# Performance work log

Measured on AMD Instinct MI355X. Metric: run time of the kernel, lower is better.

## Reference

```python
import jax, jax.numpy as jnp
import numpy as np

MARGIN = 0.2
EPS = 1e-6  # torch.pairwise_distance default eps added to (x1 - x2)


def setup_inputs() -> dict:
    key = jax.random.key(0)
    k1, k2 = jax.random.split(key)
    N, D = 8192, 128
    x = jax.random.normal(k1, (N, D), dtype=jnp.float32)
    target = jax.random.randint(k2, (N,), 0, 1000)
    return {"x": x, "target": target}


def _pairwise_dist(x):
    # torch.pairwise_distance(x.unsqueeze(0), x.unsqueeze(1)):
    #   diff[i, j] = x[j] - x[i] + EPS ; dist[i, j] = ||diff[i, j]||_2
    # Expanded quadratic form avoids the [N, N, D] diff tensor:
    #   ||a - b + e||^2 = ||a||^2 + ||b||^2 - 2 a.b + 2e*sum(a - b) + D*e^2
    sq = jnp.sum(x * x, axis=1)          # [N]
    s = jnp.sum(x, axis=1)               # [N]
    dot = x @ x.T                        # [N, N]
    D = x.shape[1]
    d2 = (sq[None, :] + sq[:, None] - 2.0 * dot
          + 2.0 * EPS * (s[None, :] - s[:, None]) + D * EPS * EPS)
    return jnp.sqrt(jnp.maximum(d2, 0.0))


def reference(x, target):
    N = x.shape[0]
    dist = _pairwise_dist(x)                                 # [N, N]
    same = target[None, :] == target[:, None]                # [N, N] bool
    pos_mask = (same & ~jnp.eye(N, dtype=bool)).astype(x.dtype)
    hardest_pos = jnp.max(pos_mask * dist, axis=1, keepdims=True)  # [N, 1]
    neg_mask = (~same).astype(x.dtype)
    max_neg = jnp.max(dist, axis=1, keepdims=True)           # [N, 1]
    anchor_neg = dist + max_neg * (1.0 - neg_mask)           # push positives up
    hardest_neg = jnp.min(anchor_neg, axis=1, keepdims=True) # [N, 1]
    loss = jax.nn.relu(hardest_pos - hardest_neg + MARGIN)
    return jnp.mean(loss)
```

## Files before the change

kernel.cpp:

```cpp
#include <hip/hip_runtime.h>

#define N 8192
#define Dk 128
#define EPSC 1e-6f
#define MARGIN 0.2f

typedef __attribute__((ext_vector_type(8))) short bf16x8;
typedef __attribute__((ext_vector_type(4))) float f32x4;

__device__ __forceinline__ unsigned short f2bf(float f) {
    unsigned u = __float_as_uint(f);
    u = (u + 0x7FFFu + ((u >> 16) & 1u)) >> 16;
    return (unsigned short)u;
}
__device__ __forceinline__ unsigned enc(float f) {
    unsigned u = __float_as_uint(f);
    return (u & 0x80000000u) ? ~u : (u | 0x80000000u);
}
__device__ __forceinline__ float dec(unsigned u) {
    return __uint_as_float((u & 0x80000000u) ? (u & 0x7FFFFFFFu) : ~u);
}

__global__ void prep_kernel(const float* __restrict__ x, const int* __restrict__ tgt,
                            unsigned short* __restrict__ Xb, uint2* __restrict__ QT,
                            float* __restrict__ P,
                            unsigned* __restrict__ wsHp, unsigned* __restrict__ wsMn) {
    int row = blockIdx.x * 4 + (threadIdx.x >> 6);
    int l = threadIdx.x & 63;
    const float2 v = *reinterpret_cast<const float2*>(&x[row * Dk + l * 2]);
    float sq = fmaf(v.x, v.x, v.y * v.y);
    float s = v.x + v.y;
    ushort2 a;
    a.x = f2bf(v.x);
    a.y = f2bf(v.y);
    *reinterpret_cast<ushort2*>(&Xb[row * Dk + l * 2]) = a;
#pragma unroll
    for (int m = 32; m >= 1; m >>= 1) {
        sq += __shfl_xor(sq, m);
        s += __shfl_xor(s, m);
    }
    if (l == 0) {
        P[row] = sq - 2.0f * EPSC * s;
        float Qj = sq + 2.0f * EPSC * s + (float)Dk * EPSC * EPSC;
        uint2 qt;
        qt.x = __float_as_uint(-0.5f * Qj);
        qt.y = (unsigned)tgt[row];
        QT[row] = qt;
        wsHp[row] = 0xFF800000u;
        wsMn[row] = 0x007FFFFFu;
    }
}

__global__ __launch_bounds__(256, 2) void main_kernel(
        const unsigned short* __restrict__ Xb,
        const uint2* __restrict__ QT, const int* __restrict__ tgt,
        unsigned* __restrict__ wsHp, unsigned* __restrict__ wsMn) {
    const int tid = threadIdx.x;
    const int w = tid >> 6;
    const int lane = tid & 63;
    const int n = lane & 15;
    const int q = lane >> 4;
    const int wi = w >> 1;
    const int wj = w & 1;

    const int ig = (int)blockIdx.x >> 3;
    const int js = (int)blockIdx.x & 7;
    const int rbase = ig * 128 + 64 * wi;

    const bf16x8* Xv = reinterpret_cast<const bf16x8*>(Xb);

    bf16x8 Af[4][4];
#pragma unroll
    for (int ti = 0; ti < 4; ++ti)
#pragma unroll
        for (int kk = 0; kk < 4; ++kk)
            Af[ti][kk] = Xv[(rbase + 16 * ti + n) * 16 + (q + 4 * kk)];

    int tsl[16];
#pragma unroll
    for (int ti = 0; ti < 4; ++ti) {
        int4 t4 = *reinterpret_cast<const int4*>(&tgt[rbase + 16 * ti + 4 * q]);
        tsl[4 * ti + 0] = t4.x;
        tsl[4 * ti + 1] = t4.y;
        tsl[4 * ti + 2] = t4.z;
        tsl[4 * ti + 3] = t4.w;
    }

    float hp[16], mn[16];
#pragma unroll
    for (int s = 0; s < 16; ++s) {
        hp[s] = INFINITY;
        mn[s] = -INFINITY;
    }

    for (int step = 0; step < 8; ++step) {
        const int jbase = js * 1024 + step * 128;

        float Qv[4];
        int tv[4];
#pragma unroll
        for (int tj = 0; tj < 4; ++tj) {
            uint2 qt = QT[jbase + 64 * wj + 16 * tj + n];
            Qv[tj] = __uint_as_float(qt.x);
            tv[tj] = (int)qt.y;
        }

        f32x4 acc[4][4];
#pragma unroll
        for (int ti = 0; ti < 4; ++ti)
#pragma unroll
            for (int tj = 0; tj < 4; ++tj) acc[ti][tj] = Qv[tj];

#pragma unroll
        for (int kk = 0; kk < 4; ++kk) {
            bf16x8 Bf[4];
#pragma unroll
            for (int tj = 0; tj < 4; ++tj)
                Bf[tj] = Xv[(jbase + 64 * wj + 16 * tj + n) * 16 + (q + 4 * kk)];
#pragma unroll
            for (int ti = 0; ti < 4; ++ti)
#pragma unroll
                for (int tj = 0; tj < 4; ++tj)
                    acc[ti][tj] = __builtin_amdgcn_mfma_f32_16x16x32_bf16(Af[ti][kk], Bf[tj],
                                                                          acc[ti][tj], 0, 0, 0);
        }

#pragma unroll
        for (int tj = 0; tj < 4; ++tj) {
            int tvv = tv[tj];
#pragma unroll
            for (int ti = 0; ti < 4; ++ti) {
                f32x4 v = acc[ti][tj];
                int e0 = tvv == tsl[4 * ti + 0];
                int e1 = tvv == tsl[4 * ti + 1];
                int e2 = tvv == tsl[4 * ti + 2];
                int e3 = tvv == tsl[4 * ti + 3];
                if (__ballot(e0 | e1 | e2 | e3)) {
                    hp[4 * ti + 0] = fminf(hp[4 * ti + 0], e0 ? v[0] : INFINITY);
                    hp[4 * ti + 1] = fminf(hp[4 * ti + 1], e1 ? v[1] : INFINITY);
                    hp[4 * ti + 2] = fminf(hp[4 * ti + 2], e2 ? v[2] : INFINITY);
                    hp[4 * ti + 3] = fminf(hp[4 * ti + 3], e3 ? v[3] : INFINITY);
                    mn[4 * ti + 0] = fmaxf(mn[4 * ti + 0], e0 ? -INFINITY : v[0]);
                    mn[4 * ti + 1] = fmaxf(mn[4 * ti + 1], e1 ? -INFINITY : v[1]);
                    mn[4 * ti + 2] = fmaxf(mn[4 * ti + 2], e2 ? -INFINITY : v[2]);
                    mn[4 * ti + 3] = fmaxf(mn[4 * ti + 3], e3 ? -INFINITY : v[3]);
                } else {
                    mn[4 * ti + 0] = fmaxf(mn[4 * ti + 0], v[0]);
                    mn[4 * ti + 1] = fmaxf(mn[4 * ti + 1], v[1]);
                    mn[4 * ti + 2] = fmaxf(mn[4 * ti + 2], v[2]);
                    mn[4 * ti + 3] = fmaxf(mn[4 * ti + 3], v[3]);
                }
            }
        }
    }

#pragma unroll
    for (int m = 1; m <= 8; m <<= 1) {
#pragma unroll
        for (int s = 0; s < 16; ++s) {
            hp[s] = fminf(hp[s], __shfl_xor(hp[s], m));
            mn[s] = fmaxf(mn[s], __shfl_xor(mn[s], m));
        }
    }
    if (n == 0) {
#pragma unroll
        for (int ti = 0; ti < 4; ++ti) {
#pragma unroll
            for (int r = 0; r < 4; ++r) {
                int i = rbase + 16 * ti + 4 * q + r;
                atomicMin(&wsHp[i], enc(hp[4 * ti + r]));
                atomicMax(&wsMn[i], enc(mn[4 * ti + r]));
            }
        }
    }
}

__global__ void finish_kernel(const float* __restrict__ P,
                              const unsigned* __restrict__ wsHp,
                              const unsigned* __restrict__ wsMn,
                              float* __restrict__ out) {
    int t = threadIdx.x;
    float sum = 0.0f;
#pragma unroll
    for (int k = 0; k < 8; ++k) {
        int i = t + 1024 * k;
        float Pi = P[i];
        float hp = sqrtf(fmaxf(fmaf(-2.0f, dec(wsHp[i]), Pi), 0.0f));
        float hn = sqrtf(fmaxf(fmaf(-2.0f, dec(wsMn[i]), Pi), 0.0f));
        sum += fmaxf(hp - hn + MARGIN, 0.0f);
    }
#pragma unroll
    for (int m = 32; m >= 1; m >>= 1) sum += __shfl_xor(sum, m);
    __shared__ float ws[16];
    if ((t & 63) == 0) ws[t >> 6] = sum;
    __syncthreads();
    if (t == 0) {
        float tot = 0.0f;
#pragma unroll
        for (int i = 0; i < 16; ++i) tot += ws[i];
        out[0] = tot * (1.0f / (float)N);
    }
}

extern "C" void kernel_launch(void* const* d_in, const int* in_sizes, int n_in,
                              void* d_out, int out_size, void* d_ws, size_t ws_size,
                              hipStream_t stream) {
    const float* x = (const float*)d_in[0];
    const int* tgt = (const int*)d_in[1];
    float* out = (float*)d_out;

    char* ws = (char*)d_ws;
    const size_t xb = (size_t)N * Dk * 2;
    unsigned short* Xb = (unsigned short*)ws;
    uint2* QT = (uint2*)(ws + xb);
    float* P = (float*)(ws + xb + (size_t)N * 8);
    unsigned* wsHp = (unsigned*)(ws + xb + (size_t)N * 12);
    unsigned* wsMn = (unsigned*)(ws + xb + (size_t)N * 16);

    prep_kernel<<<N / 4, 256, 0, stream>>>(x, tgt, Xb, QT, P, wsHp, wsMn);
    main_kernel<<<512, 256, 0, stream>>>(Xb, QT, tgt, wsHp, wsMn);
    finish_kernel<<<1, 1024, 0, stream>>>(P, wsHp, wsMn, out);
}
```

Measured before the change: 110.9 us.

## Stage B tiles into swizzled LDS via async global_load_lds double buffering

The main kernel now copies each 128-row B tile and its Q/target values into double-buffered shared memory using direct global-to-LDS loads, so the next tile is prefetched while the current one is being computed. The bf16 copy of X is written in an XOR-swizzled column order so the LDS fragment reads avoid bank conflicts, and the A fragment loads are adjusted to match. The finish kernel switches to vectorized float4 loads. The change adds 64 KB of LDS per block plus per-step barriers, which may limit occupancy under the 2-blocks-per-CU launch bound.

New measurement: 98.70 us. -11.0%, faster.

```diff
diff --git a/kernel.cpp b/kernel.cpp
--- a/kernel.cpp
+++ b/kernel.cpp
@@ -19,6 +19,12 @@
 }
 __device__ __forceinline__ float dec(unsigned u) {
     return __uint_as_float((u & 0x80000000u) ? (u & 0x7FFFFFFFu) : ~u);
+}
+
+__device__ __forceinline__ void gl_lds16(const void* src, void* lds_dst) {
+    __builtin_amdgcn_global_load_lds(
+        (const __attribute__((address_space(1))) unsigned*)src,
+        (__attribute__((address_space(3))) unsigned*)lds_dst, 16, 0, 0);
 }
 
 __global__ void prep_kernel(const float* __restrict__ x, const int* __restrict__ tgt,
@@ -33,7 +39,8 @@
     ushort2 a;
     a.x = f2bf(v.x);
     a.y = f2bf(v.y);
-    *reinterpret_cast<ushort2*>(&Xb[row * Dk + l * 2]) = a;
+    int c_phys = (l >> 2) ^ (row & 7);
+    *reinterpret_cast<ushort2*>(&Xb[row * Dk + c_phys * 8 + 2 * (l & 3)]) = a;
 #pragma unroll
     for (int m = 32; m >= 1; m >>= 1) {
         sq += __shfl_xor(sq, m);
@@ -55,6 +62,9 @@
         const unsigned short* __restrict__ Xb,
         const uint2* __restrict__ QT, const int* __restrict__ tgt,
         unsigned* __restrict__ wsHp, unsigned* __restrict__ wsMn) {
+    __shared__ unsigned short Bs[2][128 * Dk];
+    __shared__ uint2 QTs[2][128];
+
     const int tid = threadIdx.x;
     const int w = tid >> 6;
     const int lane = tid & 63;
@@ -62,6 +72,7 @@
     const int q = lane >> 4;
     const int wi = w >> 1;
     const int wj = w & 1;
+    const int sw = n & 7;
 
     const int ig = (int)blockIdx.x >> 3;
     const int js = (int)blockIdx.x & 7;
@@ -74,7 +85,7 @@
     for (int ti = 0; ti < 4; ++ti)
 #pragma unroll
         for (int kk = 0; kk < 4; ++kk)
-            Af[ti][kk] = Xv[(rbase + 16 * ti + n) * 16 + (q + 4 * kk)];
+            Af[ti][kk] = Xv[(rbase + 16 * ti + n) * 16 + ((q + 4 * kk) ^ sw)];
 
     int tsl[16];
 #pragma unroll
@@ -93,14 +104,30 @@
         mn[s] = -INFINITY;
     }
 
+    auto stage = [&](int step) {
+        const int jb = js * 1024 + step * 128;
+        const int buf = step & 1;
+#pragma unroll
+        for (int t = 0; t < 8; ++t)
+            gl_lds16(&Xb[(jb + 32 * w + 4 * t) * Dk] + lane * 8,
+                     &Bs[buf][(32 * w + 4 * t) * Dk]);
+        if (w == 0)
+            gl_lds16(reinterpret_cast<const unsigned short*>(&QT[jb]) + lane * 8,
+                     &QTs[buf][0]);
+    };
+
+    stage(0);
+
     for (int step = 0; step < 8; ++step) {
-        const int jbase = js * 1024 + step * 128;
+        const int buf = step & 1;
+        __syncthreads();
+        if (step < 7) stage(step + 1);
 
         float Qv[4];
         int tv[4];
 #pragma unroll
         for (int tj = 0; tj < 4; ++tj) {
-            uint2 qt = QT[jbase + 64 * wj + 16 * tj + n];
+            uint2 qt = QTs[buf][64 * wj + 16 * tj + n];
             Qv[tj] = __uint_as_float(qt.x);
             tv[tj] = (int)qt.y;
         }
@@ -116,7 +143,8 @@
             bf16x8 Bf[4];
 #pragma unroll
             for (int tj = 0; tj < 4; ++tj)
-                Bf[tj] = Xv[(jbase + 64 * wj + 16 * tj + n) * 16 + (q + 4 * kk)];
+                Bf[tj] = *reinterpret_cast<const bf16x8*>(
+                    &Bs[buf][(64 * wj + 16 * tj + n) * Dk + (((q + 4 * kk) ^ sw) << 3)]);
 #pragma unroll
             for (int ti = 0; ti < 4; ++ti)
 #pragma unroll
@@ -182,12 +210,20 @@
     int t = threadIdx.x;
     float sum = 0.0f;
 #pragma unroll
-    for (int k = 0; k < 8; ++k) {
-        int i = t + 1024 * k;
-        float Pi = P[i];
-        float hp = sqrtf(fmaxf(fmaf(-2.0f, dec(wsHp[i]), Pi), 0.0f));
-        float hn = sqrtf(fmaxf(fmaf(-2.0f, dec(wsMn[i]), Pi), 0.0f));
-        sum += fmaxf(hp - hn + MARGIN, 0.0f);
+    for (int h = 0; h < 2; ++h) {
+        int base = 8 * t + 4 * h;
+        float4 Pv = *reinterpret_cast<const float4*>(&P[base]);
+        uint4 Hv = *reinterpret_cast<const uint4*>(&wsHp[base]);
+        uint4 Mv = *reinterpret_cast<const uint4*>(&wsMn[base]);
+        const float* Pf = &Pv.x;
+        const unsigned* Hu = &Hv.x;
+        const unsigned* Mu = &Mv.x;
+#pragma unroll
+        for (int k = 0; k < 4; ++k) {
+            float hp = sqrtf(fmaxf(fmaf(-2.0f, dec(Hu[k]), Pf[k]), 0.0f));
+            float hn = sqrtf(fmaxf(fmaf(-2.0f, dec(Mu[k]), Pf[k]), 0.0f));
+            sum += fmaxf(hp - hn + MARGIN, 0.0f);
+        }
     }
 #pragma unroll
     for (int m = 32; m >= 1; m >>= 1) sum += __shfl_xor(sum, m);
```

## Pre-swizzle bf16 MFMA fragments, double-buffer B loads, replace atomics with partial buffers

Applied to the files above, without the earlier changes.

The prep kernel now writes bf16 data already in MFMA fragment order, so each lane loads its fragments contiguously. The main kernel changes its tiling to 64 rows per block, with each wave handling 16 columns per tile, and double-buffers the B fragments to overlap loads with MFMA. It launches 1024 blocks with a launch bound of three blocks per SM. Per-row atomic min/max on encoded floats is replaced by writes into 32 partial buffers, which the single-block finish kernel reduces. That finish kernel now reads 32x more data serially, which may add latency.

After: 191.5 us. +72.6%, slower.

```diff
diff --git a/kernel.cpp b/kernel.cpp
--- a/kernel.cpp
+++ b/kernel.cpp
@@ -13,68 +13,66 @@
     u = (u + 0x7FFFu + ((u >> 16) & 1u)) >> 16;
     return (unsigned short)u;
 }
-__device__ __forceinline__ unsigned enc(float f) {
-    unsigned u = __float_as_uint(f);
-    return (u & 0x80000000u) ? ~u : (u | 0x80000000u);
-}
-__device__ __forceinline__ float dec(unsigned u) {
-    return __uint_as_float((u & 0x80000000u) ? (u & 0x7FFFFFFFu) : ~u);
-}
 
 __global__ void prep_kernel(const float* __restrict__ x, const int* __restrict__ tgt,
-                            unsigned short* __restrict__ Xb, uint2* __restrict__ QT,
-                            float* __restrict__ P,
-                            unsigned* __restrict__ wsHp, unsigned* __restrict__ wsMn) {
-    int row = blockIdx.x * 4 + (threadIdx.x >> 6);
-    int l = threadIdx.x & 63;
-    const float2 v = *reinterpret_cast<const float2*>(&x[row * Dk + l * 2]);
-    float sq = fmaf(v.x, v.x, v.y * v.y);
-    float s = v.x + v.y;
-    ushort2 a;
-    a.x = f2bf(v.x);
-    a.y = f2bf(v.y);
-    *reinterpret_cast<ushort2*>(&Xb[row * Dk + l * 2]) = a;
-#pragma unroll
-    for (int m = 32; m >= 1; m >>= 1) {
+                            uint4* __restrict__ Frag, uint2* __restrict__ QT,
+                            float* __restrict__ P) {
+    int wv = blockIdx.x * 4 + (threadIdx.x >> 6);
+    int lane = threadIdx.x & 63;
+    int row = wv * 4 + (lane >> 4);
+    int c = lane & 15;
+    const float4* x4 = reinterpret_cast<const float4*>(x);
+    float4 v0 = x4[row * 32 + c * 2];
+    float4 v1 = x4[row * 32 + c * 2 + 1];
+    float sq = v0.x * v0.x + v0.y * v0.y + v0.z * v0.z + v0.w * v0.w +
+               v1.x * v1.x + v1.y * v1.y + v1.z * v1.z + v1.w * v1.w;
+    float s = v0.x + v0.y + v0.z + v0.w + v1.x + v1.y + v1.z + v1.w;
+    ushort4 lo, hi;
+    lo.x = f2bf(v0.x); lo.y = f2bf(v0.y); lo.z = f2bf(v0.z); lo.w = f2bf(v0.w);
+    hi.x = f2bf(v1.x); hi.y = f2bf(v1.y); hi.z = f2bf(v1.z); hi.w = f2bf(v1.w);
+    uint4 pk;
+    pk.x = (unsigned)lo.x | ((unsigned)lo.y << 16);
+    pk.y = (unsigned)lo.z | ((unsigned)lo.w << 16);
+    pk.z = (unsigned)hi.x | ((unsigned)hi.y << 16);
+    pk.w = (unsigned)hi.z | ((unsigned)hi.w << 16);
+    Frag[((row >> 4) * 4 + (c >> 2)) * 64 + (c & 3) * 16 + (row & 15)] = pk;
+#pragma unroll
+    for (int m = 1; m <= 8; m <<= 1) {
         sq += __shfl_xor(sq, m);
         s += __shfl_xor(s, m);
     }
-    if (l == 0) {
+    if (c == 0) {
         P[row] = sq - 2.0f * EPSC * s;
         float Qj = sq + 2.0f * EPSC * s + (float)Dk * EPSC * EPSC;
         uint2 qt;
         qt.x = __float_as_uint(-0.5f * Qj);
         qt.y = (unsigned)tgt[row];
         QT[row] = qt;
-        wsHp[row] = 0xFF800000u;
-        wsMn[row] = 0x007FFFFFu;
-    }
-}
-
-__global__ __launch_bounds__(256, 2) void main_kernel(
-        const unsigned short* __restrict__ Xb,
-        const uint2* __restrict__ QT, const int* __restrict__ tgt,
-        unsigned* __restrict__ wsHp, unsigned* __restrict__ wsMn) {
-    const int tid = threadIdx.x;
-    const int w = tid >> 6;
-    const int lane = tid & 63;
+    }
+}
+
+__global__ __launch_bounds__(256, 3) void main_kernel(
+        const uint4* __restrict__ Frag, const uint2* __restrict__ QT,
+        const int* __restrict__ tgt,
+        float* __restrict__ partHp, float* __restrict__ partMn) {
+    const int w = threadIdx.x >> 6;
+    const int lane = threadIdx.x & 63;
     const int n = lane & 15;
     const int q = lane >> 4;
-    const int wi = w >> 1;
-    const int wj = w & 1;
 
     const int ig = (int)blockIdx.x >> 3;
-    const int js = (int)blockIdx.x & 7;
-    const int rbase = ig * 128 + 64 * wi;
-
-    const bf16x8* Xv = reinterpret_cast<const bf16x8*>(Xb);
+    const int jg = (int)blockIdx.x & 7;
+    const int rbase = ig * 64;
+    const int jt0 = jg * 64 + w * 16;
+
+    const bf16x8* Fr = reinterpret_cast<const bf16x8*>(Frag);
 
     bf16x8 Af[4][4];
 #pragma unroll
     for (int ti = 0; ti < 4; ++ti)
 #pragma unroll
         for (int kk = 0; kk < 4; ++kk)
-            Af[ti][kk] = Xv[(rbase + 16 * ti + n) * 16 + (q + 4 * kk)];
+            Af[ti][kk] = Fr[((ig * 4 + ti) * 4 + kk) * 64 + lane];
 
     int tsl[16];
 #pragma unroll
@@ -93,65 +91,60 @@
         mn[s] = -INFINITY;
     }
 
-    for (int step = 0; step < 8; ++step) {
-        const int jbase = js * 1024 + step * 128;
-
-        float Qv[4];
-        int tv[4];
-#pragma unroll
-        for (int tj = 0; tj < 4; ++tj) {
-            uint2 qt = QT[jbase + 64 * wj + 16 * tj + n];
-            Qv[tj] = __uint_as_float(qt.x);
-            tv[tj] = (int)qt.y;
-        }
-
-        f32x4 acc[4][4];
-#pragma unroll
-        for (int ti = 0; ti < 4; ++ti)
-#pragma unroll
-            for (int tj = 0; tj < 4; ++tj) acc[ti][tj] = Qv[tj];
-
-#pragma unroll
-        for (int kk = 0; kk < 4; ++kk) {
-            bf16x8 Bf[4];
-#pragma unroll
-            for (int tj = 0; tj < 4; ++tj)
-                Bf[tj] = Xv[(jbase + 64 * wj + 16 * tj + n) * 16 + (q + 4 * kk)];
+    bf16x8 B0[4], B1[4];
+    uint2 q0, q1;
+
+    auto loadB = [&](bf16x8* B, uint2& qt, int t) {
+        const int jt = jt0 + t;
+#pragma unroll
+        for (int kk = 0; kk < 4; ++kk) B[kk] = Fr[(jt * 4 + kk) * 64 + lane];
+        qt = QT[jt * 16 + n];
+    };
+
+    auto compute = [&](const bf16x8* B, uint2 qt) {
+        const float Qv = __uint_as_float(qt.x);
+        const int tv = (int)qt.y;
+        f32x4 acc[4];
+#pragma unroll
+        for (int ti = 0; ti < 4; ++ti) acc[ti] = Qv;
+#pragma unroll
+        for (int kk = 0; kk < 4; ++kk)
 #pragma unroll
             for (int ti = 0; ti < 4; ++ti)
-#pragma unroll
-                for (int tj = 0; tj < 4; ++tj)
-                    acc[ti][tj] = __builtin_amdgcn_mfma_f32_16x16x32_bf16(Af[ti][kk], Bf[tj],
-                                                                          acc[ti][tj], 0, 0, 0);
-        }
-
-#pragma unroll
-        for (int tj = 0; tj < 4; ++tj) {
-            int tvv = tv[tj];
-#pragma unroll
-            for (int ti = 0; ti < 4; ++ti) {
-                f32x4 v = acc[ti][tj];
-                int e0 = tvv == tsl[4 * ti + 0];
-                int e1 = tvv == tsl[4 * ti + 1];
-                int e2 = tvv == tsl[4 * ti + 2];
-                int e3 = tvv == tsl[4 * ti + 3];
-                if (__ballot(e0 | e1 | e2 | e3)) {
-                    hp[4 * ti + 0] = fminf(hp[4 * ti + 0], e0 ? v[0] : INFINITY);
-                    hp[4 * ti + 1] = fminf(hp[4 * ti + 1], e1 ? v[1] : INFINITY);
-                    hp[4 * ti + 2] = fminf(hp[4 * ti + 2], e2 ? v[2] : INFINITY);
-                    hp[4 * ti + 3] = fminf(hp[4 * ti + 3], e3 ? v[3] : INFINITY);
-                    mn[4 * ti + 0] = fmaxf(mn[4 * ti + 0], e0 ? -INFINITY : v[0]);
-                    mn[4 * ti + 1] = fmaxf(mn[4 * ti + 1], e1 ? -INFINITY : v[1]);
-                    mn[4 * ti + 2] = fmaxf(mn[4 * ti + 2], e2 ? -INFINITY : v[2]);
-                    mn[4 * ti + 3] = fmaxf(mn[4 * ti + 3], e3 ? -INFINITY : v[3]);
-                } else {
-                    mn[4 * ti + 0] = fmaxf(mn[4 * ti + 0], v[0]);
-                    mn[4 * ti + 1] = fmaxf(mn[4 * ti + 1], v[1]);
-                    mn[4 * ti + 2] = fmaxf(mn[4 * ti + 2], v[2]);
-                    mn[4 * ti + 3] = fmaxf(mn[4 * ti + 3], v[3]);
-                }
+                acc[ti] = __builtin_amdgcn_mfma_f32_16x16x32_bf16(Af[ti][kk], B[kk],
+                                                                  acc[ti], 0, 0, 0);
+#pragma unroll
+        for (int ti = 0; ti < 4; ++ti) {
+            f32x4 v = acc[ti];
+            int e0 = tv == tsl[4 * ti + 0];
+            int e1 = tv == tsl[4 * ti + 1];
+            int e2 = tv == tsl[4 * ti + 2];
+            int e3 = tv == tsl[4 * ti + 3];
+            if (__ballot(e0 | e1 | e2 | e3)) {
+                hp[4 * ti + 0] = fminf(hp[4 * ti + 0], e0 ? v[0] : INFINITY);
+                hp[4 * ti + 1] = fminf(hp[4 * ti + 1], e1 ? v[1] : INFINITY);
+                hp[4 * ti + 2] = fminf(hp[4 * ti + 2], e2 ? v[2] : INFINITY);
+                hp[4 * ti + 3] = fminf(hp[4 * ti + 3], e3 ? v[3] : INFINITY);
+                mn[4 * ti + 0] = fmaxf(mn[4 * ti + 0], e0 ? -INFINITY : v[0]);
+                mn[4 * ti + 1] = fmaxf(mn[4 * ti + 1], e1 ? -INFINITY : v[1]);
+                mn[4 * ti + 2] = fmaxf(mn[4 * ti + 2], e2 ? -INFINITY : v[2]);
+                mn[4 * ti + 3] = fmaxf(mn[4 * ti + 3], e3 ? -INFINITY : v[3]);
+            } else {
+                mn[4 * ti + 0] = fmaxf(mn[4 * ti + 0], v[0]);
+                mn[4 * ti + 1] = fmaxf(mn[4 * ti + 1], v[1]);
+                mn[4 * ti + 2] = fmaxf(mn[4 * ti + 2], v[2]);
+                mn[4 * ti + 3] = fmaxf(mn[4 * ti + 3], v[3]);
             }
         }
+    };
+
+    loadB(B0, q0, 0);
+#pragma unroll
+    for (int tt = 0; tt < 16; tt += 2) {
+        if (tt + 1 < 16) loadB(B1, q1, tt + 1);
+        compute(B0, q0);
+        if (tt + 2 < 16) loadB(B0, q0, tt + 2);
+        if (tt + 1 < 16) compute(B1, q1);
     }
 
 #pragma unroll
@@ -163,30 +156,36 @@
         }
     }
     if (n == 0) {
-#pragma unroll
-        for (int ti = 0; ti < 4; ++ti) {
+        const int wg = jg * 4 + w;
+#pragma unroll
+        for (int ti = 0; ti < 4; ++ti)
 #pragma unroll
             for (int r = 0; r < 4; ++r) {
                 int i = rbase + 16 * ti + 4 * q + r;
-                atomicMin(&wsHp[i], enc(hp[4 * ti + r]));
-                atomicMax(&wsMn[i], enc(mn[4 * ti + r]));
+                partHp[wg * N + i] = hp[4 * ti + r];
+                partMn[wg * N + i] = mn[4 * ti + r];
             }
-        }
     }
 }
 
 __global__ void finish_kernel(const float* __restrict__ P,
-                              const unsigned* __restrict__ wsHp,
-                              const unsigned* __restrict__ wsMn,
+                              const float* __restrict__ partHp,
+                              const float* __restrict__ partMn,
                               float* __restrict__ out) {
     int t = threadIdx.x;
     float sum = 0.0f;
 #pragma unroll
     for (int k = 0; k < 8; ++k) {
         int i = t + 1024 * k;
+        float hpm = INFINITY, mnm = -INFINITY;
+#pragma unroll
+        for (int wg = 0; wg < 32; ++wg) {
+            hpm = fminf(hpm, partHp[wg * N + i]);
+            mnm = fmaxf(mnm, partMn[wg * N + i]);
+        }
         float Pi = P[i];
-        float hp = sqrtf(fmaxf(fmaf(-2.0f, dec(wsHp[i]), Pi), 0.0f));
-        float hn = sqrtf(fmaxf(fmaf(-2.0f, dec(wsMn[i]), Pi), 0.0f));
+        float hp = sqrtf(fmaxf(fmaf(-2.0f, hpm, Pi), 0.0f));
+        float hn = sqrtf(fmaxf(fmaf(-2.0f, mnm, Pi), 0.0f));
         sum += fmaxf(hp - hn + MARGIN, 0.0f);
     }
 #pragma unroll
@@ -210,14 +209,14 @@
     float* out = (float*)d_out;
 
     char* ws = (char*)d_ws;
-    const size_t xb = (size_t)N * Dk * 2;
-    unsigned short* Xb = (unsigned short*)ws;
-    uint2* QT = (uint2*)(ws + xb);
-    float* P = (float*)(ws + xb + (size_t)N * 8);
-    unsigned* wsHp = (unsigned*)(ws + xb + (size_t)N * 12);
-    unsigned* wsMn = (unsigned*)(ws + xb + (size_t)N * 16);
-
-    prep_kernel<<<N / 4, 256, 0, stream>>>(x, tgt, Xb, QT, P, wsHp, wsMn);
-    main_kernel<<<512, 256, 0, stream>>>(Xb, QT, tgt, wsHp, wsMn);
-    finish_kernel<<<1, 1024, 0, stream>>>(P, wsHp, wsMn, out);
-}
+    const size_t frag_b = (size_t)N * Dk * 2;
+    uint4* Frag = (uint4*)ws;
+    uint2* QT = (uint2*)(ws + frag_b);
+    float* P = (float*)(ws + frag_b + (size_t)N * 8);
+    float* partHp = (float*)(ws + frag_b + (size_t)N * 12);
+    float* partMn = (float*)(ws + frag_b + (size_t)N * 12 + (size_t)32 * N * 4);
+
+    prep_kernel<<<N / 16, 256, 0, stream>>>(x, tgt, Frag, QT, P);
+    main_kernel<<<1024, 256, 0, stream>>>(Frag, QT, tgt, partHp, partMn);
+    finish_kernel<<<1, 1024, 0, stream>>>(P, partHp, partMn, out);
+}
```
